# Kernel optimization log

Measured on AMD Instinct MI355X. Metric: run time of the kernel, lower is better.

Reference implementation:

```python
import jax, jax.numpy as jnp
import numpy as np

NUM_HEADS = 16  # matches init_kwargs num_heads


def setup_inputs() -> dict:
    key = jax.random.key(0)
    k0, k1, k2, k3, k4 = jax.random.split(key, 5)
    B, p, C = 8, 64, 1024
    N = p * p
    s = 1.0 / np.sqrt(C).astype(np.float32)
    return {
        "x": jax.random.normal(k0, (B, 3, N, C), jnp.float32),
        "wq": jax.random.normal(k1, (C, C), jnp.float32) * s,
        "wk": jax.random.normal(k2, (C, C), jnp.float32) * s,
        "wv": jax.random.normal(k3, (C, C), jnp.float32) * s,
        "w_proj": jax.random.normal(k4, (C, C), jnp.float32) * s,
        "b_proj": jnp.zeros((C,), jnp.float32),
    }


def reference(x, wq, wk, wv, w_proj, b_proj):
    # x: [B, 3, N, C] triplane tokens, N = p*p
    B, G, N, C = x.shape
    p = int(round(N ** 0.5))
    H = NUM_HEADS
    d = C // H
    scale = d ** -0.5

    xg = x.reshape(B, 3, p, p, C)
    # Linear projections are pointwise, so project each plane element once
    # (the torch code redundantly projects gathered copies; math is identical).
    qh = (xg @ wq.T).reshape(B, 3, p, p, H, d)
    kh = (xg @ wk.T).reshape(B, 3, p, p, H, d)
    vh = (xg @ wv.T).reshape(B, 3, p, p, H, d)

    outs = []
    for i in range(3):  # fixed loop over the 3 planes
        q_i = qh[:, i]                       # [B, a, j, H, d] query pixel (a, j)
        k_yz = kh[:, (i + 1) % 3]            # keys: row a of next plane -> [B, a, k, H, d]
        v_yz = vh[:, (i + 1) % 3]
        k_zx = kh[:, (i + 2) % 3]            # keys: column j of other plane -> [B, k, j, H, d]
        v_zx = vh[:, (i + 2) % 3]
        # scores against the p row-keys and p column-keys (2p keys total, 1 query)
        s1 = jnp.einsum('bajhd,bakhd->bajhk', q_i, k_yz) * scale
        s2 = jnp.einsum('bajhd,bkjhd->bajhk', q_i, k_zx) * scale
        attn = jax.nn.softmax(jnp.concatenate([s1, s2], axis=-1), axis=-1)  # [B,a,j,H,2p]
        a1, a2 = attn[..., :p], attn[..., p:]
        o = (jnp.einsum('bajhk,bakhd->bajhd', a1, v_yz)
             + jnp.einsum('bajhk,bkjhd->bajhd', a2, v_zx))  # [B,a,j,H,d]
        outs.append(o.reshape(B, N, C))
    # torch buffer is filled in [plane, B, N] order then reinterpreted as [B,3,N];
    # replicate that reshape quirk faithfully.
    out = jnp.stack(outs, axis=0)            # [3, B, N, C]
    out = out @ w_proj.T + b_proj
    return out.reshape(B, 3, N, C)
```

## Files before the change

kernel.cpp:

```cpp
#include <hip/hip_runtime.h>
#include <hip/hip_bf16.h>
#include <stdint.h>
#include <type_traits>

typedef __hip_bfloat16 hbf16;
typedef short bf16x8 __attribute__((ext_vector_type(8)));
typedef float f32x4 __attribute__((ext_vector_type(4)));
typedef unsigned int u32x4 __attribute__((ext_vector_type(4)));

#define MFMA16(a, b, c) __builtin_amdgcn_mfma_f32_16x16x32_bf16((a), (b), (c), 0, 0, 0)

__device__ __forceinline__ void gload_lds16(const void* g, void* l) {
  __builtin_amdgcn_global_load_lds(
      (const __attribute__((address_space(1))) void*)g,
      (__attribute__((address_space(3))) void*)l, 16, 0, 0);
}

__device__ __forceinline__ float b2f(unsigned short u) {
  union { unsigned int u32; float f; } cv;
  cv.u32 = ((unsigned int)u) << 16;
  return cv.f;
}
__device__ __forceinline__ unsigned short f2b(float f) {
  hbf16 h = __float2bfloat16(f);
  return __builtin_bit_cast(unsigned short, h);
}

__device__ __forceinline__ int swz(int row, int col) {
  return row * 64 + (col ^ ((row & 7) << 3));
}

__global__ __launch_bounds__(256) void cvt_f32_bf16(
    const float* __restrict__ src, unsigned short* __restrict__ dst, long long n)
{
  const long long i0 = ((long long)blockIdx.x * 256 + threadIdx.x) * 8;
  const long long stride = (long long)gridDim.x * 2048;
  for (long long i = i0; i < n; i += stride) {
    const float4 a = *(const float4*)(src + i);
    const float4 b = *(const float4*)(src + i + 4);
    bf16x8 o;
    o[0] = (short)f2b(a.x); o[1] = (short)f2b(a.y);
    o[2] = (short)f2b(a.z); o[3] = (short)f2b(a.w);
    o[4] = (short)f2b(b.x); o[5] = (short)f2b(b.y);
    o[6] = (short)f2b(b.z); o[7] = (short)f2b(b.w);
    *(bf16x8*)(dst + i) = o;
  }
}

__global__ __launch_bounds__(256) void cvt4_w(
    const float* __restrict__ s0, const float* __restrict__ s1,
    const float* __restrict__ s2, const float* __restrict__ s3,
    unsigned short* __restrict__ dst)
{
  const int q = blockIdx.x >> 9;
  const float* src = (q == 0) ? s0 : (q == 1) ? s1 : (q == 2) ? s2 : s3;
  const long long i = ((long long)(blockIdx.x & 511) * 256 + threadIdx.x) * 8;
  const float4 a = *(const float4*)(src + i);
  const float4 b = *(const float4*)(src + i + 4);
  bf16x8 o;
  o[0] = (short)f2b(a.x); o[1] = (short)f2b(a.y);
  o[2] = (short)f2b(a.z); o[3] = (short)f2b(a.w);
  o[4] = (short)f2b(b.x); o[5] = (short)f2b(b.y);
  o[6] = (short)f2b(b.z); o[7] = (short)f2b(b.w);
  *(bf16x8*)(dst + (long long)q * 1048576 + i) = o;
}

__global__ __launch_bounds__(256, 3) void gemm_qkv(
    const unsigned short* __restrict__ A,
    const unsigned short* __restrict__ W,
    unsigned short* __restrict__ Cq,
    unsigned short* __restrict__ Ck,
    unsigned short* __restrict__ Cv,
    int M, int Ntot, int K)
{
  __shared__ __attribute__((aligned(16))) unsigned short Sm[24576];

  const int tid  = threadIdx.x;
  const int lane = tid & 63;
  const int w    = tid >> 6;
  const int wr   = w >> 1;
  const int wc   = w & 1;
  const int lr   = lane & 15;
  const int lg   = lane >> 4;

  const int bx    = blockIdx.x;
  const int xcd   = bx & 7;
  const int idx   = bx >> 3;
  const int tileN = xcd * 3 + idx % 3;
  const int tileM = idx / 3;
  const size_t rowBase = (size_t)tileM * 256;
  const int    colBase = tileN * 128;

  const int sRow   = tid >> 2;
  const int sChunk = (tid & 3) ^ ((tid >> 3) & 3);
  const unsigned short* Ag0 = A + (rowBase +   0 + sRow) * (size_t)K + sChunk * 8;
  const unsigned short* Ag1 = A + (rowBase +  64 + sRow) * (size_t)K + sChunk * 8;
  const unsigned short* Ag2 = A + (rowBase + 128 + sRow) * (size_t)K + sChunk * 8;
  const unsigned short* Ag3 = A + (rowBase + 192 + sRow) * (size_t)K + sChunk * 8;
  const unsigned short* Wg0 = W + ((size_t)colBase +  0 + sRow) * K + sChunk * 8;
  const unsigned short* Wg1 = W + ((size_t)colBase + 64 + sRow) * K + sChunk * 8;

  f32x4 acc[8][4] = {};
  const int nt = K >> 5;

  {
    unsigned short* ab = Sm;
    unsigned short* bb = Sm + 16384;
    gload_lds16(Ag0, ab +        w * 512);
    gload_lds16(Ag1, ab + 2048 + w * 512);
    gload_lds16(Ag2, ab + 4096 + w * 512);
    gload_lds16(Ag3, ab + 6144 + w * 512);
    gload_lds16(Wg0, bb +        w * 512);
    gload_lds16(Wg1, bb + 2048 + w * 512);
  }

#define QITER(T, STG)                                                         \
  do {                                                                        \
    asm volatile("s_waitcnt vmcnt(0)" ::: "memory");                          \
    __builtin_amdgcn_s_barrier();                                             \
    __builtin_amdgcn_sched_barrier(0);                                        \
    if (STG) {                                                                \
      const int nb = ((T) + 1) & 1;                                           \
      const size_t ke = (size_t)((T) + 1) * 32;                               \
      unsigned short* ab = Sm + nb * 8192;                                    \
      unsigned short* bb = Sm + 16384 + nb * 4096;                            \
      gload_lds16(Ag0 + ke, ab +        w * 512);                             \
      gload_lds16(Ag1 + ke, ab + 2048 + w * 512);                             \
      gload_lds16(Ag2 + ke, ab + 4096 + w * 512);                             \
      gload_lds16(Ag3 + ke, ab + 6144 + w * 512);                             \
      gload_lds16(Wg0 + ke, bb +        w * 512);                             \
      gload_lds16(Wg1 + ke, bb + 2048 + w * 512);                             \
    }                                                                         \
    const unsigned short* asb = Sm + ((T) & 1) * 8192;                        \
    const unsigned short* bsb = Sm + 16384 + ((T) & 1) * 4096;                \
    bf16x8 af[8], bfv[4];                                                     \
    _Pragma("unroll")                                                         \
    for (int mi = 0; mi < 8; ++mi) {                                          \
      const int row = wr * 128 + mi * 16 + lr;                                \
      af[mi] = *(const bf16x8*)(asb + row * 32 + (lg ^ ((row >> 1) & 3)) * 8);\
    }                                                                         \
    _Pragma("unroll")                                                         \
    for (int ni = 0; ni < 4; ++ni) {                                          \
      const int row = wc * 64 + ni * 16 + lr;                                 \
      bfv[ni] = *(const bf16x8*)(bsb + row * 32 + (lg ^ ((row >> 1) & 3)) * 8);\
    }                                                                         \
    _Pragma("unroll")                                                         \
    for (int mi = 0; mi < 8; ++mi)                                            \
      _Pragma("unroll")                                                       \
      for (int ni = 0; ni < 4; ++ni)                                          \
        acc[mi][ni] = MFMA16(af[mi], bfv[ni], acc[mi][ni]);                   \
  } while (0)

  for (int t = 0; t < nt - 1; ++t) QITER(t, true);
  QITER(nt - 1, false);
#undef QITER

  __syncthreads();
  const int out = colBase >> 10;
  unsigned short* Co = (out == 0) ? Cq : (out == 1) ? Ck : Cv;
  const int colLocal = colBase & 1023;
  unsigned short* G = Sm + wr * 8192;

#pragma unroll
  for (int half = 0; half < 2; ++half) {
#pragma unroll
    for (int mi2 = 0; mi2 < 4; ++mi2) {
      const int mi = half * 4 + mi2;
#pragma unroll
      for (int ni = 0; ni < 4; ++ni)
#pragma unroll
        for (int r = 0; r < 4; ++r) {
          const int row = mi2 * 16 + lg * 4 + r;
          const int c   = wc * 64 + ni * 16 + lr;
          G[row * 128 + (c ^ (((row >> 2) & 3) << 4))] = f2b(acc[mi][ni][r]);
        }
    }
    __syncthreads();
#pragma unroll
    for (int it = 0; it < 8; ++it) {
      const int ch  = it * 128 + wc * 64 + lane;
      const int row = ch >> 4, cc = ch & 15;
      const u32x4 v = *(const u32x4*)(G + row * 128 + ((cc * 8) ^ (((row >> 2) & 3) << 4)));
      *(u32x4*)(Co + (rowBase + wr * 128 + half * 64 + row) * 1024 + colLocal + cc * 8) = v;
    }
    __syncthreads();
  }
}

__global__ __launch_bounds__(256, 3) void gemm_proj(
    const unsigned short* __restrict__ A,
    const unsigned short* __restrict__ W,
    const float* __restrict__ bias,
    float* __restrict__ C,
    int M, int N, int K)
{
  __shared__ __attribute__((aligned(16))) unsigned short Sm[24576];

  const int tid  = threadIdx.x;
  const int lane = tid & 63;
  const int w    = tid >> 6;
  const int wr   = w >> 1;
  const int wc   = w & 1;
  const int lr   = lane & 15;
  const int lg   = lane >> 4;

  const int nwg     = gridDim.x;
  const int bx      = blockIdx.x;
  const int logical = (bx & 7) * (nwg >> 3) + (bx >> 3);
  const int colsN   = N >> 7;
  const int tileM   = logical / colsN;
  const int tileN   = logical - tileM * colsN;
  const size_t rowBase = (size_t)tileM * 256;
  const int    colBase = tileN * 128;

  const int sRow   = tid >> 2;
  const int sChunk = (tid & 3) ^ ((tid >> 3) & 3);
  const unsigned short* Ag0 = A + (rowBase +   0 + sRow) * (size_t)K + sChunk * 8;
  const unsigned short* Ag1 = A + (rowBase +  64 + sRow) * (size_t)K + sChunk * 8;
  const unsigned short* Ag2 = A + (rowBase + 128 + sRow) * (size_t)K + sChunk * 8;
  const unsigned short* Ag3 = A + (rowBase + 192 + sRow) * (size_t)K + sChunk * 8;
  const unsigned short* Wg0 = W + ((size_t)colBase +  0 + sRow) * K + sChunk * 8;
  const unsigned short* Wg1 = W + ((size_t)colBase + 64 + sRow) * K + sChunk * 8;

  f32x4 acc[8][4] = {};
  const int nt = K >> 5;

  {
    unsigned short* ab = Sm;
    unsigned short* bb = Sm + 16384;
    gload_lds16(Ag0, ab +        w * 512);
    gload_lds16(Ag1, ab + 2048 + w * 512);
    gload_lds16(Ag2, ab + 4096 + w * 512);
    gload_lds16(Ag3, ab + 6144 + w * 512);
    gload_lds16(Wg0, bb +        w * 512);
    gload_lds16(Wg1, bb + 2048 + w * 512);
  }

#define PITER(T, STG)                                                         \
  do {                                                                        \
    asm volatile("s_waitcnt vmcnt(0)" ::: "memory");                          \
    __builtin_amdgcn_s_barrier();                                             \
    __builtin_amdgcn_sched_barrier(0);                                        \
    if (STG) {                                                                \
      const int nb = ((T) + 1) & 1;                                           \
      const size_t ke = (size_t)((T) + 1) * 32;                               \
      unsigned short* ab = Sm + nb * 8192;                                    \
      unsigned short* bb = Sm + 16384 + nb * 4096;                            \
      gload_lds16(Ag0 + ke, ab +        w * 512);                             \
      gload_lds16(Ag1 + ke, ab + 2048 + w * 512);                             \
      gload_lds16(Ag2 + ke, ab + 4096 + w * 512);                             \
      gload_lds16(Ag3 + ke, ab + 6144 + w * 512);                             \
      gload_lds16(Wg0 + ke, bb +        w * 512);                             \
      gload_lds16(Wg1 + ke, bb + 2048 + w * 512);                             \
    }                                                                         \
    const unsigned short* asb = Sm + ((T) & 1) * 8192;                        \
    const unsigned short* bsb = Sm + 16384 + ((T) & 1) * 4096;                \
    bf16x8 af[8], bfv[4];                                                     \
    _Pragma("unroll")                                                         \
    for (int mi = 0; mi < 8; ++mi) {                                          \
      const int row = wr * 128 + mi * 16 + lr;                                \
      af[mi] = *(const bf16x8*)(asb + row * 32 + (lg ^ ((row >> 1) & 3)) * 8);\
    }                                                                         \
    _Pragma("unroll")                                                         \
    for (int ni = 0; ni < 4; ++ni) {                                          \
      const int row = wc * 64 + ni * 16 + lr;                                 \
      bfv[ni] = *(const bf16x8*)(bsb + row * 32 + (lg ^ ((row >> 1) & 3)) * 8);\
    }                                                                         \
    _Pragma("unroll")                                                         \
    for (int mi = 0; mi < 8; ++mi)                                            \
      _Pragma("unroll")                                                       \
      for (int ni = 0; ni < 4; ++ni)                                          \
        acc[mi][ni] = MFMA16(af[mi], bfv[ni], acc[mi][ni]);                   \
  } while (0)

  for (int t = 0; t < nt - 1; ++t) PITER(t, true);
  PITER(nt - 1, false);
#undef PITER

  __syncthreads();

  float bv[4];
#pragma unroll
  for (int ni = 0; ni < 4; ++ni)
    bv[ni] = bias ? bias[colBase + wc * 64 + ni * 16 + lr] : 0.0f;

  float* G = (float*)(void*)Sm + wr * 4096;

#pragma unroll
  for (int batch = 0; batch < 4; ++batch) {
#pragma unroll
    for (int mi2 = 0; mi2 < 2; ++mi2) {
      const int mi = batch * 2 + mi2;
#pragma unroll
      for (int ni = 0; ni < 4; ++ni)
#pragma unroll
        for (int r = 0; r < 4; ++r) {
          const int row = mi2 * 16 + lg * 4 + r;
          const int c   = wc * 64 + ni * 16 + lr;
          G[row * 128 + (c ^ (((row >> 2) & 3) << 4))] = acc[mi][ni][r] + bv[ni];
        }
    }
    __syncthreads();
#pragma unroll
    for (int it = 0; it < 8; ++it) {
      const int ch  = it * 128 + wc * 64 + lane;
      const int row = ch >> 5, cc = ch & 31;
      const float4 v = *(const float4*)(G + row * 128 + ((cc * 4) ^ (((row >> 2) & 3) << 4)));
      *(float4*)(C + (rowBase + wr * 128 + batch * 32 + row) * (size_t)N + colBase + cc * 4) = v;
    }
    __syncthreads();
  }
}

__global__ __launch_bounds__(256) void attn_yz(
    const unsigned short* __restrict__ Q,
    const unsigned short* __restrict__ Kx,
    const unsigned short* __restrict__ Vx,
    unsigned short* __restrict__ O1,
    float* __restrict__ m1s, float* __restrict__ l1s)
{
  __shared__ __attribute__((aligned(16))) unsigned short Qs[4096], Ks[4096], Vs[4096], Ps[4096];

  const int bid = blockIdx.x;
  const int h = bid & 15;
  const int a = (bid >> 4) & 63;
  const int b = (bid >> 10) & 7;
  const int i = bid >> 13;
  const int i1 = (i + 1) % 3;

  const size_t qoff = ((size_t)((b * 3 + i) * 4096 + a * 64)) * 1024 + h * 64;
  const size_t koff = ((size_t)((b * 3 + i1) * 4096 + a * 64)) * 1024 + h * 64;

  const int tid = threadIdx.x;
#pragma unroll
  for (int it = 0; it < 2; ++it) {
    const int idx = it * 2048 + tid * 8;
    const int row = idx >> 6, col = idx & 63;
    const int d = swz(row, col);
    *(bf16x8*)&Qs[d] = *(const bf16x8*)(Q + qoff + (size_t)row * 1024 + col);
    *(bf16x8*)&Ks[d] = *(const bf16x8*)(Kx + koff + (size_t)row * 1024 + col);
    *(bf16x8*)&Vs[d] = *(const bf16x8*)(Vx + koff + (size_t)row * 1024 + col);
  }
  __syncthreads();

  const int lane = tid & 63;
  const int w  = tid >> 6;
  const int lr = lane & 15;
  const int lg = lane >> 4;

  f32x4 sa[4] = {};
  {
    const bf16x8 aq0 = *(const bf16x8*)&Qs[swz(w * 16 + lr, lg * 8)];
    const bf16x8 aq1 = *(const bf16x8*)&Qs[swz(w * 16 + lr, 32 + lg * 8)];
#pragma unroll
    for (int nf = 0; nf < 4; ++nf) {
      const bf16x8 bk0 = *(const bf16x8*)&Ks[swz(nf * 16 + lr, lg * 8)];
      const bf16x8 bk1 = *(const bf16x8*)&Ks[swz(nf * 16 + lr, 32 + lg * 8)];
      sa[nf] = MFMA16(aq0, bk0, sa[nf]);
      sa[nf] = MFMA16(aq1, bk1, sa[nf]);
    }
  }

  const float scale = 0.125f;
  float m[4], ls[4];
#pragma unroll
  for (int r = 0; r < 4; ++r) {
#pragma unroll
    for (int nf = 0; nf < 4; ++nf) sa[nf][r] *= scale;
    float v = fmaxf(fmaxf(sa[0][r], sa[1][r]), fmaxf(sa[2][r], sa[3][r]));
    v = fmaxf(v, __shfl_xor(v, 1));
    v = fmaxf(v, __shfl_xor(v, 2));
    v = fmaxf(v, __shfl_xor(v, 4));
    v = fmaxf(v, __shfl_xor(v, 8));
    m[r] = v;
    float s = 0.0f;
#pragma unroll
    for (int nf = 0; nf < 4; ++nf) { const float p = __expf(sa[nf][r] - v); sa[nf][r] = p; s += p; }
    s += __shfl_xor(s, 1);
    s += __shfl_xor(s, 2);
    s += __shfl_xor(s, 4);
    s += __shfl_xor(s, 8);
    ls[r] = s;
  }

#pragma unroll
  for (int nf = 0; nf < 4; ++nf)
#pragma unroll
    for (int r = 0; r < 4; ++r)
      Ps[swz(w * 16 + lg * 4 + r, nf * 16 + lr)] = f2b(sa[nf][r]);

  if (lr == 0) {
    const size_t sb = ((size_t)(i * 8 + b) * 16 + h) * 4096 + a * 64 + w * 16 + lg * 4;
#pragma unroll
    for (int r = 0; r < 4; ++r) { m1s[sb + r] = m[r]; l1s[sb + r] = ls[r]; }
  }
  __syncthreads();

  f32x4 oa[4] = {};
#pragma unroll
  for (int ks = 0; ks < 2; ++ks) {
    const bf16x8 ap = *(const bf16x8*)&Ps[swz(w * 16 + lr, ks * 32 + lg * 8)];
#pragma unroll
    for (int df = 0; df < 4; ++df) {
      bf16x8 bv;
#pragma unroll
      for (int e = 0; e < 8; ++e)
        bv[e] = (short)Vs[swz(ks * 32 + lg * 8 + e, df * 16 + lr)];
      oa[df] = MFMA16(ap, bv, oa[df]);
    }
  }

  const size_t ob = ((size_t)(i * 8 + b) * 4096 + a * 64) * 1024 + h * 64;
#pragma unroll
  for (int df = 0; df < 4; ++df)
#pragma unroll
    for (int r = 0; r < 4; ++r)
      O1[ob + (size_t)(w * 16 + lg * 4 + r) * 1024 + df * 16 + lr] = f2b(oa[df][r]);
}

__global__ __launch_bounds__(256) void attn_zx(
    const unsigned short* __restrict__ Q,
    const unsigned short* __restrict__ Kx,
    const unsigned short* __restrict__ Vx,
    unsigned short* __restrict__ O1,
    const float* __restrict__ m1s, const float* __restrict__ l1s)
{
  __shared__ __attribute__((aligned(16))) unsigned short Qs[4096], Ks[4096], Vs[4096], Ps[4096];

  const int bid = blockIdx.x;
  const int j = bid & 63;
  const int h = (bid >> 6) & 15;
  const int b = (bid >> 10) & 7;
  const int i = bid >> 13;
  const int i2 = (i + 2) % 3;

  const size_t qoff = ((size_t)(b * 3 + i) * 4096 + j) * 1024 + h * 64;
  const size_t koff = ((size_t)(b * 3 + i2) * 4096 + j) * 1024 + h * 64;
  const size_t rstride = 65536;

  const int tid = threadIdx.x;
#pragma unroll
  for (int it = 0; it < 2; ++it) {
    const int idx = it * 2048 + tid * 8;
    const int row = idx >> 6, col = idx & 63;
    const int d = swz(row, col);
    *(bf16x8*)&Qs[d] = *(const bf16x8*)(Q + qoff + (size_t)row * rstride + col);
    *(bf16x8*)&Ks[d] = *(const bf16x8*)(Kx + koff + (size_t)row * rstride + col);
    *(bf16x8*)&Vs[d] = *(const bf16x8*)(Vx + koff + (size_t)row * rstride + col);
  }
  __syncthreads();

  const int lane = tid & 63;
  const int w  = tid >> 6;
  const int lr = lane & 15;
  const int lg = lane >> 4;

  f32x4 sa[4] = {};
  {
    const bf16x8 aq0 = *(const bf16x8*)&Qs[swz(w * 16 + lr, lg * 8)];
    const bf16x8 aq1 = *(const bf16x8*)&Qs[swz(w * 16 + lr, 32 + lg * 8)];
#pragma unroll
    for (int nf = 0; nf < 4; ++nf) {
      const bf16x8 bk0 = *(const bf16x8*)&Ks[swz(nf * 16 + lr, lg * 8)];
      const bf16x8 bk1 = *(const bf16x8*)&Ks[swz(nf * 16 + lr, 32 + lg * 8)];
      sa[nf] = MFMA16(aq0, bk0, sa[nf]);
      sa[nf] = MFMA16(aq1, bk1, sa[nf]);
    }
  }

  const float scale = 0.125f;
  float m[4], ls[4];
#pragma unroll
  for (int r = 0; r < 4; ++r) {
#pragma unroll
    for (int nf = 0; nf < 4; ++nf) sa[nf][r] *= scale;
    float v = fmaxf(fmaxf(sa[0][r], sa[1][r]), fmaxf(sa[2][r], sa[3][r]));
    v = fmaxf(v, __shfl_xor(v, 1));
    v = fmaxf(v, __shfl_xor(v, 2));
    v = fmaxf(v, __shfl_xor(v, 4));
    v = fmaxf(v, __shfl_xor(v, 8));
    m[r] = v;
    float s = 0.0f;
#pragma unroll
    for (int nf = 0; nf < 4; ++nf) { const float p = __expf(sa[nf][r] - v); sa[nf][r] = p; s += p; }
    s += __shfl_xor(s, 1);
    s += __shfl_xor(s, 2);
    s += __shfl_xor(s, 4);
    s += __shfl_xor(s, 8);
    ls[r] = s;
  }

  float c1[4], c2[4], rden[4];
  const size_t sb = ((size_t)(i * 8 + b) * 16 + h) * 4096 + j;
#pragma unroll
  for (int r = 0; r < 4; ++r) {
    const int arow = w * 16 + lg * 4 + r;
    const float mm1 = m1s[sb + (size_t)arow * 64];
    const float ll1 = l1s[sb + (size_t)arow * 64];
    const float mm = fmaxf(mm1, m[r]);
    const float e1 = __expf(mm1 - mm);
    const float e2 = __expf(m[r] - mm);
    c1[r] = e1; c2[r] = e2;
    rden[r] = 1.0f / (e1 * ll1 + e2 * ls[r]);
  }

#pragma unroll
  for (int nf = 0; nf < 4; ++nf)
#pragma unroll
    for (int r = 0; r < 4; ++r)
      Ps[swz(w * 16 + lg * 4 + r, nf * 16 + lr)] = f2b(sa[nf][r]);
  __syncthreads();

  f32x4 oa[4] = {};
#pragma unroll
  for (int ks = 0; ks < 2; ++ks) {
    const bf16x8 ap = *(const bf16x8*)&Ps[swz(w * 16 + lr, ks * 32 + lg * 8)];
#pragma unroll
    for (int df = 0; df < 4; ++df) {
      bf16x8 bv;
#pragma unroll
      for (int e = 0; e < 8; ++e)
        bv[e] = (short)Vs[swz(ks * 32 + lg * 8 + e, df * 16 + lr)];
      oa[df] = MFMA16(ap, bv, oa[df]);
    }
  }

  const size_t ob = ((size_t)(i * 8 + b) * 4096 + j) * 1024 + h * 64;
#pragma unroll
  for (int df = 0; df < 4; ++df)
#pragma unroll
    for (int r = 0; r < 4; ++r) {
      const size_t addr = ob + (size_t)(w * 16 + lg * 4 + r) * rstride + df * 16 + lr;
      const float o1v = b2f(O1[addr]);
      O1[addr] = f2b((c1[r] * o1v + c2[r] * oa[df][r]) * rden[r]);
    }
}

extern "C" void kernel_launch(void* const* d_in, const int* in_sizes, int n_in,
                              void* d_out, int out_size, void* d_ws, size_t ws_size,
                              hipStream_t stream)
{
  const float* x  = (const float*)d_in[0];
  const float* wq = (const float*)d_in[1];
  const float* wk = (const float*)d_in[2];
  const float* wv = (const float*)d_in[3];
  const float* wp = (const float*)d_in[4];
  const float* bp = (const float*)d_in[5];

  const int M = 98304, N = 1024, K = 1024;
  const size_t SLAB = 201326592ull;
  const size_t STAT = 6291456ull;

  char* ws = (char*)d_ws;
  unsigned short* xb  = (unsigned short*)(ws);
  unsigned short* Kb  = (unsigned short*)(ws + SLAB);
  unsigned short* Vb  = (unsigned short*)(ws + 2 * SLAB);
  float* m1s          = (float*)(ws + 3 * SLAB);
  float* l1s          = (float*)(ws + 3 * SLAB + STAT);
  unsigned short* wqb = (unsigned short*)(ws + 3 * SLAB + 2 * STAT);
  unsigned short* wpb = wqb + 3145728;
  unsigned short* Qb  = (unsigned short*)d_out;
  unsigned short* O1  = xb;

  dim3 blk(256);
  cvt_f32_bf16<<<dim3(4096), blk, 0, stream>>>(x, xb, (long long)M * 1024);
  cvt4_w<<<dim3(2048), blk, 0, stream>>>(wq, wk, wv, wp, wqb);

  gemm_qkv<<<dim3((M / 256) * (3072 / 128)), dim3(256), 0, stream>>>(
      xb, wqb, Qb, Kb, Vb, M, 3072, K);

  attn_yz<<<dim3(24576), blk, 0, stream>>>(Qb, Kb, Vb, O1, m1s, l1s);
  attn_zx<<<dim3(24576), blk, 0, stream>>>(Qb, Kb, Vb, O1, m1s, l1s);

  gemm_proj<<<dim3((M / 256) * (N / 128)), dim3(256), 0, stream>>>(
      O1, wpb, bp, (float*)d_out, M, N, K);
}
```

Baseline: 1.422 ms.

## Triple-buffer LDS in QKV and projection GEMMs with deeper prefetch

```diff
diff --git a/kernel.cpp b/kernel.cpp
--- a/kernel.cpp
+++ b/kernel.cpp
@@ -65,7 +65,7 @@
   *(bf16x8*)(dst + (long long)q * 1048576 + i) = o;
 }
 
-__global__ __launch_bounds__(256, 3) void gemm_qkv(
+__global__ __launch_bounds__(256, 2) void gemm_qkv(
     const unsigned short* __restrict__ A,
     const unsigned short* __restrict__ W,
     unsigned short* __restrict__ Cq,
@@ -73,7 +73,7 @@
     unsigned short* __restrict__ Cv,
     int M, int Ntot, int K)
 {
-  __shared__ __attribute__((aligned(16))) unsigned short Sm[24576];
+  __shared__ __attribute__((aligned(16))) unsigned short Sm[36864];
 
   const int tid  = threadIdx.x;
   const int lane = tid & 63;
@@ -103,27 +103,29 @@
   f32x4 acc[8][4] = {};
   const int nt = K >> 5;
 
-  {
-    unsigned short* ab = Sm;
-    unsigned short* bb = Sm + 16384;
-    gload_lds16(Ag0, ab +        w * 512);
-    gload_lds16(Ag1, ab + 2048 + w * 512);
-    gload_lds16(Ag2, ab + 4096 + w * 512);
-    gload_lds16(Ag3, ab + 6144 + w * 512);
-    gload_lds16(Wg0, bb +        w * 512);
-    gload_lds16(Wg1, bb + 2048 + w * 512);
-  }
-
-#define QITER(T, STG)                                                         \
+#pragma unroll
+  for (int p = 0; p < 2; ++p) {
+    const size_t ke = (size_t)p * 32;
+    unsigned short* ab = Sm + p * 8192;
+    unsigned short* bb = Sm + 24576 + p * 4096;
+    gload_lds16(Ag0 + ke, ab +        w * 512);
+    gload_lds16(Ag1 + ke, ab + 2048 + w * 512);
+    gload_lds16(Ag2 + ke, ab + 4096 + w * 512);
+    gload_lds16(Ag3 + ke, ab + 6144 + w * 512);
+    gload_lds16(Wg0 + ke, bb +        w * 512);
+    gload_lds16(Wg1 + ke, bb + 2048 + w * 512);
+  }
+
+#define QITER(T, VM, STG)                                                     \
   do {                                                                        \
-    asm volatile("s_waitcnt vmcnt(0)" ::: "memory");                          \
+    asm volatile("s_waitcnt vmcnt(" VM ")" ::: "memory");                     \
     __builtin_amdgcn_s_barrier();                                             \
     __builtin_amdgcn_sched_barrier(0);                                        \
     if (STG) {                                                                \
-      const int nb = ((T) + 1) & 1;                                           \
-      const size_t ke = (size_t)((T) + 1) * 32;                               \
+      const int nb = ((T) + 2) % 3;                                           \
+      const size_t ke = (size_t)((T) + 2) * 32;                               \
       unsigned short* ab = Sm + nb * 8192;                                    \
-      unsigned short* bb = Sm + 16384 + nb * 4096;                            \
+      unsigned short* bb = Sm + 24576 + nb * 4096;                            \
       gload_lds16(Ag0 + ke, ab +        w * 512);                             \
       gload_lds16(Ag1 + ke, ab + 2048 + w * 512);                             \
       gload_lds16(Ag2 + ke, ab + 4096 + w * 512);                             \
@@ -131,8 +133,8 @@
       gload_lds16(Wg0 + ke, bb +        w * 512);                             \
       gload_lds16(Wg1 + ke, bb + 2048 + w * 512);                             \
     }                                                                         \
-    const unsigned short* asb = Sm + ((T) & 1) * 8192;                        \
-    const unsigned short* bsb = Sm + 16384 + ((T) & 1) * 4096;                \
+    const unsigned short* asb = Sm + ((T) % 3) * 8192;                        \
+    const unsigned short* bsb = Sm + 24576 + ((T) % 3) * 4096;                \
     bf16x8 af[8], bfv[4];                                                     \
     _Pragma("unroll")                                                         \
     for (int mi = 0; mi < 8; ++mi) {                                          \
@@ -151,50 +153,45 @@
         acc[mi][ni] = MFMA16(af[mi], bfv[ni], acc[mi][ni]);                   \
   } while (0)
 
-  for (int t = 0; t < nt - 1; ++t) QITER(t, true);
-  QITER(nt - 1, false);
+  for (int t = 0; t < nt - 2; ++t) QITER(t, "6", true);
+  QITER(nt - 2, "6", false);
+  QITER(nt - 1, "0", false);
 #undef QITER
 
   __syncthreads();
+  unsigned short* G = Sm + wr * 16384;
+#pragma unroll
+  for (int mi = 0; mi < 8; ++mi)
+#pragma unroll
+    for (int ni = 0; ni < 4; ++ni)
+#pragma unroll
+      for (int r = 0; r < 4; ++r) {
+        const int row = mi * 16 + lg * 4 + r;
+        const int c   = wc * 64 + ni * 16 + lr;
+        G[row * 128 + (c ^ (((row >> 2) & 3) << 4))] = f2b(acc[mi][ni][r]);
+      }
+  __syncthreads();
+
   const int out = colBase >> 10;
   unsigned short* Co = (out == 0) ? Cq : (out == 1) ? Ck : Cv;
   const int colLocal = colBase & 1023;
-  unsigned short* G = Sm + wr * 8192;
-
-#pragma unroll
-  for (int half = 0; half < 2; ++half) {
-#pragma unroll
-    for (int mi2 = 0; mi2 < 4; ++mi2) {
-      const int mi = half * 4 + mi2;
-#pragma unroll
-      for (int ni = 0; ni < 4; ++ni)
-#pragma unroll
-        for (int r = 0; r < 4; ++r) {
-          const int row = mi2 * 16 + lg * 4 + r;
-          const int c   = wc * 64 + ni * 16 + lr;
-          G[row * 128 + (c ^ (((row >> 2) & 3) << 4))] = f2b(acc[mi][ni][r]);
-        }
-    }
-    __syncthreads();
-#pragma unroll
-    for (int it = 0; it < 8; ++it) {
-      const int ch  = it * 128 + wc * 64 + lane;
-      const int row = ch >> 4, cc = ch & 15;
-      const u32x4 v = *(const u32x4*)(G + row * 128 + ((cc * 8) ^ (((row >> 2) & 3) << 4)));
-      *(u32x4*)(Co + (rowBase + wr * 128 + half * 64 + row) * 1024 + colLocal + cc * 8) = v;
-    }
-    __syncthreads();
-  }
-}
-
-__global__ __launch_bounds__(256, 3) void gemm_proj(
+#pragma unroll
+  for (int it = 0; it < 16; ++it) {
+    const int ch  = it * 128 + wc * 64 + lane;
+    const int row = ch >> 4, cc = ch & 15;
+    const u32x4 v = *(const u32x4*)(G + row * 128 + ((cc * 8) ^ (((row >> 2) & 3) << 4)));
+    *(u32x4*)(Co + (rowBase + wr * 128 + row) * 1024 + colLocal + cc * 8) = v;
+  }
+}
+
+__global__ __launch_bounds__(256, 2) void gemm_proj(
     const unsigned short* __restrict__ A,
     const unsigned short* __restrict__ W,
     const float* __restrict__ bias,
     float* __restrict__ C,
     int M, int N, int K)
 {
-  __shared__ __attribute__((aligned(16))) unsigned short Sm[24576];
+  __shared__ __attribute__((aligned(16))) unsigned short Sm[36864];
 
   const int tid  = threadIdx.x;
   const int lane = tid & 63;
@@ -204,12 +201,9 @@
   const int lr   = lane & 15;
   const int lg   = lane >> 4;
 
-  const int nwg     = gridDim.x;
-  const int bx      = blockIdx.x;
-  const int logical = (bx & 7) * (nwg >> 3) + (bx >> 3);
-  const int colsN   = N >> 7;
-  const int tileM   = logical / colsN;
-  const int tileN   = logical - tileM * colsN;
+  const int bx    = blockIdx.x;
+  const int tileN = bx & 7;
+  const int tileM = bx >> 3;
   const size_t rowBase = (size_t)tileM * 256;
   const int    colBase = tileN * 128;
 
@@ -225,27 +219,29 @@
   f32x4 acc[8][4] = {};
   const int nt = K >> 5;
 
-  {
-    unsigned short* ab = Sm;
-    unsigned short* bb = Sm + 16384;
-    gload_lds16(Ag0, ab +        w * 512);
-    gload_lds16(Ag1, ab + 2048 + w * 512);
-    gload_lds16(Ag2, ab + 4096 + w * 512);
-    gload_lds16(Ag3, ab + 6144 + w * 512);
-    gload_lds16(Wg0, bb +        w * 512);
-    gload_lds16(Wg1, bb + 2048 + w * 512);
-  }
-
-#define PITER(T, STG)                                                         \
+#pragma unroll
+  for (int p = 0; p < 2; ++p) {
+    const size_t ke = (size_t)p * 32;
+    unsigned short* ab = Sm + p * 8192;
+    unsigned short* bb = Sm + 24576 + p * 4096;
+    gload_lds16(Ag0 + ke, ab +        w * 512);
+    gload_lds16(Ag1 + ke, ab + 2048 + w * 512);
+    gload_lds16(Ag2 + ke, ab + 4096 + w * 512);
+    gload_lds16(Ag3 + ke, ab + 6144 + w * 512);
+    gload_lds16(Wg0 + ke, bb +        w * 512);
+    gload_lds16(Wg1 + ke, bb + 2048 + w * 512);
+  }
+
+#define PITER(T, VM, STG)                                                     \
   do {                                                                        \
-    asm volatile("s_waitcnt vmcnt(0)" ::: "memory");                          \
+    asm volatile("s_waitcnt vmcnt(" VM ")" ::: "memory");                     \
     __builtin_amdgcn_s_barrier();                                             \
     __builtin_amdgcn_sched_barrier(0);                                        \
     if (STG) {                                                                \
-      const int nb = ((T) + 1) & 1;                                           \
-      const size_t ke = (size_t)((T) + 1) * 32;                               \
+      const int nb = ((T) + 2) % 3;                                           \
+      const size_t ke = (size_t)((T) + 2) * 32;                               \
       unsigned short* ab = Sm + nb * 8192;                                    \
-      unsigned short* bb = Sm + 16384 + nb * 4096;                            \
+      unsigned short* bb = Sm + 24576 + nb * 4096;                            \
       gload_lds16(Ag0 + ke, ab +        w * 512);                             \
       gload_lds16(Ag1 + ke, ab + 2048 + w * 512);                             \
       gload_lds16(Ag2 + ke, ab + 4096 + w * 512);                             \
@@ -253,8 +249,8 @@
       gload_lds16(Wg0 + ke, bb +        w * 512);                             \
       gload_lds16(Wg1 + ke, bb + 2048 + w * 512);                             \
     }                                                                         \
-    const unsigned short* asb = Sm + ((T) & 1) * 8192;                        \
-    const unsigned short* bsb = Sm + 16384 + ((T) & 1) * 4096;                \
+    const unsigned short* asb = Sm + ((T) % 3) * 8192;                        \
+    const unsigned short* bsb = Sm + 24576 + ((T) % 3) * 4096;                \
     bf16x8 af[8], bfv[4];                                                     \
     _Pragma("unroll")                                                         \
     for (int mi = 0; mi < 8; ++mi) {                                          \
@@ -273,8 +269,9 @@
         acc[mi][ni] = MFMA16(af[mi], bfv[ni], acc[mi][ni]);                   \
   } while (0)
 
-  for (int t = 0; t < nt - 1; ++t) PITER(t, true);
-  PITER(nt - 1, false);
+  for (int t = 0; t < nt - 2; ++t) PITER(t, "6", true);
+  PITER(nt - 2, "6", false);
+  PITER(nt - 1, "0", false);
 #undef PITER
 
   __syncthreads();
```

Result: no change. 1.448 ms (+1.8%).
